# Optimization experiments

Hardware: AMD Instinct MI355X
Metric: run time of the kernel (lower is better)

Reference implementation:

```python
import jax, jax.numpy as jnp
import numpy as np

N_NODES = 50000
N_EDGES = 800000
D_FEAT = 64


def setup_inputs() -> dict:
    key = jax.random.key(0)
    k1, k2, k3 = jax.random.split(key, 3)
    x_sum = jax.random.normal(k1, (N_NODES, D_FEAT), dtype=jnp.float32)
    x_prod = jax.random.uniform(k2, (N_NODES, D_FEAT), dtype=jnp.float32)
    edge_index = jax.random.randint(k3, (2, N_EDGES), 0, N_NODES, dtype=jnp.int64)
    return {"x_sum": x_sum, "x_prod": x_prod, "edge_index": edge_index}


def reference(x_sum, x_prod, edge_index):
    # flow='source_to_target' -> gather from edge_index[0], aggregate at edge_index[1]
    src_idx = edge_index[0]
    dst_idx = edge_index[1]
    n = x_sum.shape[0]

    # __lift__: index_select along node dim (message is identity; edge_attr/norm None)
    m_sum = x_sum[src_idx]    # [E, D]
    m_prod = x_prod[src_idx]  # [E, D]

    # scatter_sum: zeros-init + scatter_add_
    out_sum = jax.ops.segment_sum(m_sum, dst_idx, num_segments=n)

    # scatter_product: ones-init + scatter_(reduce='multiply')
    out_prod = jnp.ones((n, x_prod.shape[1]), dtype=x_prod.dtype).at[dst_idx].multiply(m_prod)

    return out_sum, out_prod
```

## Files before the change

kernel.cpp:

```cpp
#include <hip/hip_runtime.h>
#include <hip/hip_fp16.h>

#define N_NODES 50000
#define N_EDGES 800000
#define D_FEAT  64
#define BSHIFT  6
#define NBKT    782
#define NB      256
#define CHUNK   3125
#define PSHIFT  20
#define SRC_MASK ((1 << PSHIFT) - 1)

#define WS_FLAG    0
#define WS_TOT     64
#define WS_COFF    (WS_TOT + NBKT)
#define WS_BH      (WS_COFF + NBKT + 1)
#define WS_OFFS    (WS_BH + NBKT * NB)
#define WS_PAIR    (WS_OFFS + N_NODES + 1)
#define WS_SSRC    (WS_PAIR + N_EDGES)
#define WS_PACKED  (WS_SSRC + N_EDGES)
#define WS_INTS    (WS_PACKED + N_NODES * D_FEAT)

__device__ inline void detect_idx_layout(const int* idx, int* flag) {
    int allzero = 1;
    #pragma unroll
    for (int i = 1; i < 129; i += 2) {
        if (idx[i] != 0) allzero = 0;
    }
    *flag = allzero;
}

__global__ __launch_bounds__(256) void init_cast(int* __restrict__ W,
                                                 const int* __restrict__ idx,
                                                 const float* __restrict__ xs,
                                                 const float* __restrict__ xp) {
    int tid = blockIdx.x * blockDim.x + threadIdx.x;
    int stride = gridDim.x * blockDim.x;
    __half2* packed = (__half2*)(W + WS_PACKED);
    const int total = N_NODES * D_FEAT;
    for (int i = tid; i < total; i += stride)
        packed[i] = __floats2half2_rn(xs[i], xp[i]);
    if (tid == 0) {
        detect_idx_layout(idx, W + WS_FLAG);
        W[WS_OFFS + N_NODES] = N_EDGES;
    }
}

__global__ __launch_bounds__(256) void block_hist(const int* __restrict__ idx,
                                                  int* __restrict__ W) {
    __shared__ int h[NBKT];
    for (int i = threadIdx.x; i < NBKT; i += 256) h[i] = 0;
    __syncthreads();
    const int flg = W[WS_FLAG];
    const int base = blockIdx.x * CHUNK;
    for (int e = base + threadIdx.x; e < base + CHUNK; e += 256) {
        int dst = flg ? idx[2 * (N_EDGES + e)] : idx[N_EDGES + e];
        atomicAdd(&h[dst >> BSHIFT], 1);
    }
    __syncthreads();
    for (int i = threadIdx.x; i < NBKT; i += 256)
        W[WS_BH + i * NB + blockIdx.x] = h[i];
}

__global__ __launch_bounds__(256) void bucket_scan(int* __restrict__ W) {
    __shared__ int part[NB];
    int j = blockIdx.x;
    int t = threadIdx.x;
    int c = W[WS_BH + j * NB + t];
    part[t] = c;
    __syncthreads();
    for (int off = 1; off < NB; off <<= 1) {
        int u = (t >= off) ? part[t - off] : 0;
        __syncthreads();
        part[t] += u;
        __syncthreads();
    }
    W[WS_BH + j * NB + t] = part[t] - c;
    if (t == NB - 1) W[WS_TOT + j] = part[t];
}

__global__ __launch_bounds__(1024) void base_scan(int* __restrict__ W) {
    __shared__ int part[1024];
    int t = threadIdx.x;
    int v = (t < NBKT) ? W[WS_TOT + t] : 0;
    part[t] = v;
    __syncthreads();
    for (int off = 1; off < 1024; off <<= 1) {
        int u = (t >= off) ? part[t - off] : 0;
        __syncthreads();
        part[t] += u;
        __syncthreads();
    }
    if (t < NBKT) W[WS_COFF + t] = part[t] - v;
    if (t == 0) W[WS_COFF + NBKT] = N_EDGES;
}

__global__ __launch_bounds__(256) void coarse_scatter(const int* __restrict__ idx,
                                                      int* __restrict__ W) {
    __shared__ int cur[NBKT];
    for (int i = threadIdx.x; i < NBKT; i += 256)
        cur[i] = W[WS_COFF + i] + W[WS_BH + i * NB + blockIdx.x];
    __syncthreads();
    const int flg = W[WS_FLAG];
    const int base = blockIdx.x * CHUNK;
    for (int e = base + threadIdx.x; e < base + CHUNK; e += 256) {
        int src, dst;
        if (flg) { src = idx[2 * e]; dst = idx[2 * (N_EDGES + e)]; }
        else     { src = idx[e];     dst = idx[N_EDGES + e]; }
        int pos = atomicAdd(&cur[dst >> BSHIFT], 1);
        W[WS_PAIR + pos] = src | ((dst & 63) << PSHIFT);
    }
}

__global__ __launch_bounds__(256) void fine_sort(int* __restrict__ W) {
    __shared__ int h[64];
    int b = blockIdx.x;
    int t = threadIdx.x;
    int bbase = W[WS_COFF + b];
    int bend  = W[WS_COFF + b + 1];
    if (t < 64) h[t] = 0;
    __syncthreads();
    for (int e = bbase + t; e < bend; e += 256)
        atomicAdd(&h[(unsigned)W[WS_PAIR + e] >> PSHIFT], 1);
    __syncthreads();
    if (t < 64) {
        int c = h[t];
        int incl = c;
        #pragma unroll
        for (int off = 1; off < 64; off <<= 1) {
            int u = __shfl_up(incl, off, 64);
            if (t >= off) incl += u;
        }
        int excl = incl - c;
        int node = (b << BSHIFT) + t;
        if (node < N_NODES) W[WS_OFFS + node] = bbase + excl;
        h[t] = excl;
    }
    __syncthreads();
    for (int e = bbase + t; e < bend; e += 256) {
        int v = W[WS_PAIR + e];
        int p = atomicAdd(&h[(unsigned)v >> PSHIFT], 1);
        W[WS_SSRC + bbase + p] = v & SRC_MASK;
    }
}

__global__ __launch_bounds__(256) void gather_reduce(const int* __restrict__ W,
                                                     float* __restrict__ out) {
    int wave = (int)((blockIdx.x * blockDim.x + threadIdx.x) >> 6);
    int lane = threadIdx.x & 63;
    if (wave >= N_NODES) return;
    int beg = __builtin_amdgcn_readfirstlane(W[WS_OFFS + wave]);
    int end = __builtin_amdgcn_readfirstlane(W[WS_OFFS + wave + 1]);
    const int* ssrc = W + WS_SSRC;
    const __half2* packed = (const __half2*)(W + WS_PACKED);

    float s0 = 0.f, s1 = 0.f, s2 = 0.f, s3 = 0.f;
    float s4 = 0.f, s5 = 0.f, s6 = 0.f, s7 = 0.f;
    float p0 = 1.f, p1 = 1.f, p2 = 1.f, p3 = 1.f;
    float p4 = 1.f, p5 = 1.f, p6 = 1.f, p7 = 1.f;
    int i = beg;
    for (; i + 7 < end; i += 8) {
        int a0 = ssrc[i],     a1 = ssrc[i + 1], a2 = ssrc[i + 2], a3 = ssrc[i + 3];
        int a4 = ssrc[i + 4], a5 = ssrc[i + 5], a6 = ssrc[i + 6], a7 = ssrc[i + 7];
        float2 f0 = __half22float2(packed[a0 * D_FEAT + lane]);
        float2 f1 = __half22float2(packed[a1 * D_FEAT + lane]);
        float2 f2 = __half22float2(packed[a2 * D_FEAT + lane]);
        float2 f3 = __half22float2(packed[a3 * D_FEAT + lane]);
        float2 f4 = __half22float2(packed[a4 * D_FEAT + lane]);
        float2 f5 = __half22float2(packed[a5 * D_FEAT + lane]);
        float2 f6 = __half22float2(packed[a6 * D_FEAT + lane]);
        float2 f7 = __half22float2(packed[a7 * D_FEAT + lane]);
        s0 += f0.x; s1 += f1.x; s2 += f2.x; s3 += f3.x;
        s4 += f4.x; s5 += f5.x; s6 += f6.x; s7 += f7.x;
        p0 *= f0.y; p1 *= f1.y; p2 *= f2.y; p3 *= f3.y;
        p4 *= f4.y; p5 *= f5.y; p6 *= f6.y; p7 *= f7.y;
    }
    for (; i + 1 < end; i += 2) {
        int a0 = ssrc[i], a1 = ssrc[i + 1];
        float2 f0 = __half22float2(packed[a0 * D_FEAT + lane]);
        float2 f1 = __half22float2(packed[a1 * D_FEAT + lane]);
        s0 += f0.x; s1 += f1.x;
        p0 *= f0.y; p1 *= f1.y;
    }
    if (i < end) {
        float2 f = __half22float2(packed[ssrc[i] * D_FEAT + lane]);
        s0 += f.x;
        p0 *= f.y;
    }
    float ssum = ((s0 + s1) + (s2 + s3)) + ((s4 + s5) + (s6 + s7));
    float pprd = ((p0 * p1) * (p2 * p3)) * ((p4 * p5) * (p6 * p7));
    out[(long)wave * D_FEAT + lane] = ssum;
    out[(long)N_NODES * D_FEAT + (long)wave * D_FEAT + lane] = pprd;
}

__device__ inline void atomicMulF32(float* addr, float val) {
    unsigned int* ua = (unsigned int*)addr;
    unsigned int old = __hip_atomic_load(ua, __ATOMIC_RELAXED, __HIP_MEMORY_SCOPE_AGENT);
    while (true) {
        unsigned int assumed = old;
        unsigned int desired = __float_as_uint(__uint_as_float(assumed) * val);
        old = atomicCAS(ua, assumed, desired);
        if (old == assumed) break;
    }
}

__global__ void fb_init(float* __restrict__ out, int* __restrict__ flag,
                        const int* __restrict__ idx) {
    const int n4 = (N_NODES * D_FEAT) / 4;
    int tid = blockIdx.x * blockDim.x + threadIdx.x;
    int stride = gridDim.x * blockDim.x;
    float4* o = (float4*)out;
    const float4 z = make_float4(0.f, 0.f, 0.f, 0.f);
    const float4 one = make_float4(1.f, 1.f, 1.f, 1.f);
    for (int i = tid; i < n4; i += stride) { o[i] = z; o[n4 + i] = one; }
    if (blockIdx.x == 0 && threadIdx.x == 0) detect_idx_layout(idx, flag);
}

__global__ void fb_scatter(const float* __restrict__ xs, const float* __restrict__ xp,
                           const int* __restrict__ idx, float* __restrict__ out,
                           const int* __restrict__ flag) {
    long tid = (long)blockIdx.x * blockDim.x + threadIdx.x;
    const long total = (long)N_EDGES * (D_FEAT / 4);
    if (tid >= total) return;
    int e = (int)(tid >> 4);
    int c = (int)(tid & 15);
    int src, dst;
    if (*flag) { src = idx[2 * e]; dst = idx[2 * (N_EDGES + e)]; }
    else       { src = idx[e];     dst = idx[N_EDGES + e]; }
    const float4 s = ((const float4*)(xs + (long)src * D_FEAT))[c];
    const float4 p = ((const float4*)(xp + (long)src * D_FEAT))[c];
    float* os = out + (long)dst * D_FEAT + c * 4;
    float* op = out + (long)N_NODES * D_FEAT + (long)dst * D_FEAT + c * 4;
    atomicAdd(os + 0, s.x); atomicAdd(os + 1, s.y);
    atomicAdd(os + 2, s.z); atomicAdd(os + 3, s.w);
    atomicMulF32(op + 0, p.x); atomicMulF32(op + 1, p.y);
    atomicMulF32(op + 2, p.z); atomicMulF32(op + 3, p.w);
}

extern "C" void kernel_launch(void* const* d_in, const int* in_sizes, int n_in,
                              void* d_out, int out_size, void* d_ws, size_t ws_size,
                              hipStream_t stream) {
    const float* x_sum  = (const float*)d_in[0];
    const float* x_prod = (const float*)d_in[1];
    const int*   eidx   = (const int*)d_in[2];
    float* out = (float*)d_out;
    int* W = (int*)d_ws;

    if (ws_size < (size_t)WS_INTS * sizeof(int)) {
        fb_init<<<1024, 256, 0, stream>>>(out, W, eidx);
        const long total = (long)N_EDGES * (D_FEAT / 4);
        int grid = (int)((total + 255) / 256);
        fb_scatter<<<grid, 256, 0, stream>>>(x_sum, x_prod, eidx, out, W);
        return;
    }

    init_cast<<<1024, 256, 0, stream>>>(W, eidx, x_sum, x_prod);
    block_hist<<<NB, 256, 0, stream>>>(eidx, W);
    bucket_scan<<<NBKT, 256, 0, stream>>>(W);
    base_scan<<<1, 1024, 0, stream>>>(W);
    coarse_scatter<<<NB, 256, 0, stream>>>(eidx, W);
    fine_sort<<<NBKT, 256, 0, stream>>>(W);
    gather_reduce<<<(N_NODES + 3) / 4, 256, 0, stream>>>(W, out);
}
```

Baseline: 147.4 us.

## Fuse pipeline stages: cast+histogram, inline bucket scan, sort+gather in LDS

Merges the fp16 packing pass with the bucket histogram (now vectorised with float4 loads), drops the separate base_scan kernel by recomputing the bucket prefix inside coarse_scatter and sort_gather, and fuses fine sorting with the gather-reduce so each bucket's sorted source list stays in shared memory. This removes three kernel launches and a global round trip for the sorted indices and node offsets. In exchange, the cast now runs on only 256 blocks, sort_gather redundantly sums bucket totals per block, and buckets larger than CAP fall back to a slower unrolled-free global path.

```diff
diff --git a/kernel.cpp b/kernel.cpp
--- a/kernel.cpp
+++ b/kernel.cpp
@@ -10,16 +10,14 @@
 #define CHUNK   3125
 #define PSHIFT  20
 #define SRC_MASK ((1 << PSHIFT) - 1)
-
-#define WS_FLAG    0
-#define WS_TOT     64
-#define WS_COFF    (WS_TOT + NBKT)
-#define WS_BH      (WS_COFF + NBKT + 1)
-#define WS_OFFS    (WS_BH + NBKT * NB)
-#define WS_PAIR    (WS_OFFS + N_NODES + 1)
-#define WS_SSRC    (WS_PAIR + N_EDGES)
-#define WS_PACKED  (WS_SSRC + N_EDGES)
-#define WS_INTS    (WS_PACKED + N_NODES * D_FEAT)
+#define CAP     6144
+
+#define WS_TOT    0
+#define WS_BH     784
+#define WS_PAIR   (WS_BH + NBKT * NB)
+#define WS_SSRC   (WS_PAIR + N_EDGES)
+#define WS_PACKED (WS_SSRC + N_EDGES)
+#define WS_INTS   (WS_PACKED + N_NODES * D_FEAT)
 
 __device__ inline void detect_idx_layout(const int* idx, int* flag) {
     int allzero = 1;
@@ -30,35 +28,39 @@
     *flag = allzero;
 }
 
-__global__ __launch_bounds__(256) void init_cast(int* __restrict__ W,
+__global__ __launch_bounds__(256) void cast_hist(int* __restrict__ W,
                                                  const int* __restrict__ idx,
                                                  const float* __restrict__ xs,
                                                  const float* __restrict__ xp) {
-    int tid = blockIdx.x * blockDim.x + threadIdx.x;
-    int stride = gridDim.x * blockDim.x;
-    __half2* packed = (__half2*)(W + WS_PACKED);
-    const int total = N_NODES * D_FEAT;
-    for (int i = tid; i < total; i += stride)
-        packed[i] = __floats2half2_rn(xs[i], xp[i]);
-    if (tid == 0) {
-        detect_idx_layout(idx, W + WS_FLAG);
-        W[WS_OFFS + N_NODES] = N_EDGES;
-    }
-}
-
-__global__ __launch_bounds__(256) void block_hist(const int* __restrict__ idx,
-                                                  int* __restrict__ W) {
     __shared__ int h[NBKT];
-    for (int i = threadIdx.x; i < NBKT; i += 256) h[i] = 0;
-    __syncthreads();
-    const int flg = W[WS_FLAG];
+    __shared__ int flg_s;
+    const int t = threadIdx.x;
+    for (int i = t; i < NBKT; i += 256) h[i] = 0;
+    if (t == 0) detect_idx_layout(idx, &flg_s);
+    __syncthreads();
+
+    const float4* xs4 = (const float4*)xs;
+    const float4* xp4 = (const float4*)xp;
+    uint4* pk4 = (uint4*)(W + WS_PACKED);
+    union { __half2 h2; unsigned int u; } c0, c1, c2, c3;
+    const int tid = blockIdx.x * 256 + t;
+    for (int g = tid; g < (N_NODES * D_FEAT) / 4; g += NB * 256) {
+        float4 a = xs4[g], b = xp4[g];
+        c0.h2 = __floats2half2_rn(a.x, b.x);
+        c1.h2 = __floats2half2_rn(a.y, b.y);
+        c2.h2 = __floats2half2_rn(a.z, b.z);
+        c3.h2 = __floats2half2_rn(a.w, b.w);
+        pk4[g] = make_uint4(c0.u, c1.u, c2.u, c3.u);
+    }
+
+    const int flg = flg_s;
     const int base = blockIdx.x * CHUNK;
-    for (int e = base + threadIdx.x; e < base + CHUNK; e += 256) {
+    for (int e = base + t; e < base + CHUNK; e += 256) {
         int dst = flg ? idx[2 * (N_EDGES + e)] : idx[N_EDGES + e];
         atomicAdd(&h[dst >> BSHIFT], 1);
     }
     __syncthreads();
-    for (int i = threadIdx.x; i < NBKT; i += 256)
+    for (int i = t; i < NBKT; i += 256)
         W[WS_BH + i * NB + blockIdx.x] = h[i];
 }
 
@@ -79,31 +81,44 @@
     if (t == NB - 1) W[WS_TOT + j] = part[t];
 }
 
-__global__ __launch_bounds__(1024) void base_scan(int* __restrict__ W) {
-    __shared__ int part[1024];
-    int t = threadIdx.x;
-    int v = (t < NBKT) ? W[WS_TOT + t] : 0;
-    part[t] = v;
-    __syncthreads();
-    for (int off = 1; off < 1024; off <<= 1) {
-        int u = (t >= off) ? part[t - off] : 0;
-        __syncthreads();
-        part[t] += u;
-        __syncthreads();
-    }
-    if (t < NBKT) W[WS_COFF + t] = part[t] - v;
-    if (t == 0) W[WS_COFF + NBKT] = N_EDGES;
-}
-
 __global__ __launch_bounds__(256) void coarse_scatter(const int* __restrict__ idx,
                                                       int* __restrict__ W) {
     __shared__ int cur[NBKT];
-    for (int i = threadIdx.x; i < NBKT; i += 256)
-        cur[i] = W[WS_COFF + i] + W[WS_BH + i * NB + blockIdx.x];
-    __syncthreads();
-    const int flg = W[WS_FLAG];
+    __shared__ int flg_s;
+    const int t = threadIdx.x;
+    for (int i = t; i < NBKT; i += 256) cur[i] = W[WS_TOT + i];
+    if (t == 0) detect_idx_layout(idx, &flg_s);
+    __syncthreads();
+    if (t < 64) {
+        int vals[13];
+        int sum = 0;
+        const int base = t * 13;
+        #pragma unroll
+        for (int j = 0; j < 13; ++j) {
+            int k = base + j;
+            vals[j] = (k < NBKT) ? cur[k] : 0;
+            sum += vals[j];
+        }
+        int incl = sum;
+        #pragma unroll
+        for (int off = 1; off < 64; off <<= 1) {
+            int u = __shfl_up(incl, off, 64);
+            if (t >= off) incl += u;
+        }
+        int run = incl - sum;
+        #pragma unroll
+        for (int j = 0; j < 13; ++j) {
+            int k = base + j;
+            if (k < NBKT) cur[k] = run;
+            run += vals[j];
+        }
+    }
+    __syncthreads();
+    for (int i = t; i < NBKT; i += 256) cur[i] += W[WS_BH + i * NB + blockIdx.x];
+    __syncthreads();
+    const int flg = flg_s;
     const int base = blockIdx.x * CHUNK;
-    for (int e = base + threadIdx.x; e < base + CHUNK; e += 256) {
+    for (int e = base + t; e < base + CHUNK; e += 256) {
         int src, dst;
         if (flg) { src = idx[2 * e]; dst = idx[2 * (N_EDGES + e)]; }
         else     { src = idx[e];     dst = idx[N_EDGES + e]; }
@@ -112,15 +127,30 @@
     }
 }
 
-__global__ __launch_bounds__(256) void fine_sort(int* __restrict__ W) {
+__global__ __launch_bounds__(512) void sort_gather(int* __restrict__ W,
+                                                   float* __restrict__ out) {
+    __shared__ int ssrc_l[CAP];
+    __shared__ int red[512];
     __shared__ int h[64];
-    int b = blockIdx.x;
-    int t = threadIdx.x;
-    int bbase = W[WS_COFF + b];
-    int bend  = W[WS_COFF + b + 1];
+    __shared__ int noff[65];
+    const int b = blockIdx.x;
+    const int t = threadIdx.x;
+
+    int part = 0;
+    for (int k = t; k < b; k += 512) part += W[WS_TOT + k];
+    red[t] = part;
     if (t < 64) h[t] = 0;
     __syncthreads();
-    for (int e = bbase + t; e < bend; e += 256)
+    #pragma unroll
+    for (int off = 256; off > 0; off >>= 1) {
+        if (t < off) red[t] += red[t + off];
+        __syncthreads();
+    }
+    const int bbase = red[0];
+    const int bend  = bbase + W[WS_TOT + b];
+    const int nedge = bend - bbase;
+
+    for (int e = bbase + t; e < bend; e += 512)
         atomicAdd(&h[(unsigned)W[WS_PAIR + e] >> PSHIFT], 1);
     __syncthreads();
     if (t < 64) {
@@ -131,66 +161,86 @@
             int u = __shfl_up(incl, off, 64);
             if (t >= off) incl += u;
         }
-        int excl = incl - c;
-        int node = (b << BSHIFT) + t;
-        if (node < N_NODES) W[WS_OFFS + node] = bbase + excl;
-        h[t] = excl;
-    }
-    __syncthreads();
-    for (int e = bbase + t; e < bend; e += 256) {
-        int v = W[WS_PAIR + e];
-        int p = atomicAdd(&h[(unsigned)v >> PSHIFT], 1);
-        W[WS_SSRC + bbase + p] = v & SRC_MASK;
-    }
-}
-
-__global__ __launch_bounds__(256) void gather_reduce(const int* __restrict__ W,
-                                                     float* __restrict__ out) {
-    int wave = (int)((blockIdx.x * blockDim.x + threadIdx.x) >> 6);
-    int lane = threadIdx.x & 63;
-    if (wave >= N_NODES) return;
-    int beg = __builtin_amdgcn_readfirstlane(W[WS_OFFS + wave]);
-    int end = __builtin_amdgcn_readfirstlane(W[WS_OFFS + wave + 1]);
-    const int* ssrc = W + WS_SSRC;
+        noff[t] = incl - c;
+        if (t == 63) noff[64] = incl;
+        h[t] = incl - c;
+    }
+    __syncthreads();
+
+    const bool fits = (nedge <= CAP);
+    if (fits) {
+        for (int e = bbase + t; e < bend; e += 512) {
+            int v = W[WS_PAIR + e];
+            int p = atomicAdd(&h[(unsigned)v >> PSHIFT], 1);
+            ssrc_l[p] = v & SRC_MASK;
+        }
+    } else {
+        for (int e = bbase + t; e < bend; e += 512) {
+            int v = W[WS_PAIR + e];
+            int p = atomicAdd(&h[(unsigned)v >> PSHIFT], 1);
+            W[WS_SSRC + bbase + p] = v & SRC_MASK;
+        }
+    }
+    __syncthreads();
+
     const __half2* packed = (const __half2*)(W + WS_PACKED);
-
-    float s0 = 0.f, s1 = 0.f, s2 = 0.f, s3 = 0.f;
-    float s4 = 0.f, s5 = 0.f, s6 = 0.f, s7 = 0.f;
-    float p0 = 1.f, p1 = 1.f, p2 = 1.f, p3 = 1.f;
-    float p4 = 1.f, p5 = 1.f, p6 = 1.f, p7 = 1.f;
-    int i = beg;
-    for (; i + 7 < end; i += 8) {
-        int a0 = ssrc[i],     a1 = ssrc[i + 1], a2 = ssrc[i + 2], a3 = ssrc[i + 3];
-        int a4 = ssrc[i + 4], a5 = ssrc[i + 5], a6 = ssrc[i + 6], a7 = ssrc[i + 7];
-        float2 f0 = __half22float2(packed[a0 * D_FEAT + lane]);
-        float2 f1 = __half22float2(packed[a1 * D_FEAT + lane]);
-        float2 f2 = __half22float2(packed[a2 * D_FEAT + lane]);
-        float2 f3 = __half22float2(packed[a3 * D_FEAT + lane]);
-        float2 f4 = __half22float2(packed[a4 * D_FEAT + lane]);
-        float2 f5 = __half22float2(packed[a5 * D_FEAT + lane]);
-        float2 f6 = __half22float2(packed[a6 * D_FEAT + lane]);
-        float2 f7 = __half22float2(packed[a7 * D_FEAT + lane]);
-        s0 += f0.x; s1 += f1.x; s2 += f2.x; s3 += f3.x;
-        s4 += f4.x; s5 += f5.x; s6 += f6.x; s7 += f7.x;
-        p0 *= f0.y; p1 *= f1.y; p2 *= f2.y; p3 *= f3.y;
-        p4 *= f4.y; p5 *= f5.y; p6 *= f6.y; p7 *= f7.y;
-    }
-    for (; i + 1 < end; i += 2) {
-        int a0 = ssrc[i], a1 = ssrc[i + 1];
-        float2 f0 = __half22float2(packed[a0 * D_FEAT + lane]);
-        float2 f1 = __half22float2(packed[a1 * D_FEAT + lane]);
-        s0 += f0.x; s1 += f1.x;
-        p0 *= f0.y; p1 *= f1.y;
-    }
-    if (i < end) {
-        float2 f = __half22float2(packed[ssrc[i] * D_FEAT + lane]);
-        s0 += f.x;
-        p0 *= f.y;
-    }
-    float ssum = ((s0 + s1) + (s2 + s3)) + ((s4 + s5) + (s6 + s7));
-    float pprd = ((p0 * p1) * (p2 * p3)) * ((p4 * p5) * (p6 * p7));
-    out[(long)wave * D_FEAT + lane] = ssum;
-    out[(long)N_NODES * D_FEAT + (long)wave * D_FEAT + lane] = pprd;
+    const int wave = t >> 6;
+    const int lane = t & 63;
+    for (int nn = wave; nn < 64; nn += 8) {
+        const int node = (b << BSHIFT) + nn;
+        if (node >= N_NODES) break;
+        int beg = __builtin_amdgcn_readfirstlane(noff[nn]);
+        int end = __builtin_amdgcn_readfirstlane(noff[nn + 1]);
+
+        float s0 = 0.f, s1 = 0.f, s2 = 0.f, s3 = 0.f;
+        float s4 = 0.f, s5 = 0.f, s6 = 0.f, s7 = 0.f;
+        float p0 = 1.f, p1 = 1.f, p2 = 1.f, p3 = 1.f;
+        float p4 = 1.f, p5 = 1.f, p6 = 1.f, p7 = 1.f;
+        if (fits) {
+            int i = beg;
+            for (; i + 7 < end; i += 8) {
+                int a0 = ssrc_l[i],     a1 = ssrc_l[i + 1];
+                int a2 = ssrc_l[i + 2], a3 = ssrc_l[i + 3];
+                int a4 = ssrc_l[i + 4], a5 = ssrc_l[i + 5];
+                int a6 = ssrc_l[i + 6], a7 = ssrc_l[i + 7];
+                float2 f0 = __half22float2(packed[a0 * D_FEAT + lane]);
+                float2 f1 = __half22float2(packed[a1 * D_FEAT + lane]);
+                float2 f2 = __half22float2(packed[a2 * D_FEAT + lane]);
+                float2 f3 = __half22float2(packed[a3 * D_FEAT + lane]);
+                float2 f4 = __half22float2(packed[a4 * D_FEAT + lane]);
+                float2 f5 = __half22float2(packed[a5 * D_FEAT + lane]);
+                float2 f6 = __half22float2(packed[a6 * D_FEAT + lane]);
+                float2 f7 = __half22float2(packed[a7 * D_FEAT + lane]);
+                s0 += f0.x; s1 += f1.x; s2 += f2.x; s3 += f3.x;
+                s4 += f4.x; s5 += f5.x; s6 += f6.x; s7 += f7.x;
+                p0 *= f0.y; p1 *= f1.y; p2 *= f2.y; p3 *= f3.y;
+                p4 *= f4.y; p5 *= f5.y; p6 *= f6.y; p7 *= f7.y;
+            }
+            for (; i + 1 < end; i += 2) {
+                int a0 = ssrc_l[i], a1 = ssrc_l[i + 1];
+                float2 f0 = __half22float2(packed[a0 * D_FEAT + lane]);
+                float2 f1 = __half22float2(packed[a1 * D_FEAT + lane]);
+                s0 += f0.x; s1 += f1.x;
+                p0 *= f0.y; p1 *= f1.y;
+            }
+            if (i < end) {
+                float2 f = __half22float2(packed[ssrc_l[i] * D_FEAT + lane]);
+                s0 += f.x;
+                p0 *= f.y;
+            }
+        } else {
+            for (int i = beg; i < end; ++i) {
+                int a = W[WS_SSRC + bbase + i];
+                float2 f = __half22float2(packed[a * D_FEAT + lane]);
+                s0 += f.x;
+                p0 *= f.y;
+            }
+        }
+        float ssum = ((s0 + s1) + (s2 + s3)) + ((s4 + s5) + (s6 + s7));
+        float pprd = ((p0 * p1) * (p2 * p3)) * ((p4 * p5) * (p6 * p7));
+        out[(long)node * D_FEAT + lane] = ssum;
+        out[(long)N_NODES * D_FEAT + (long)node * D_FEAT + lane] = pprd;
+    }
 }
 
 __device__ inline void atomicMulF32(float* addr, float val) {
@@ -254,11 +304,8 @@
         return;
     }
 
-    init_cast<<<1024, 256, 0, stream>>>(W, eidx, x_sum, x_prod);
-    block_hist<<<NB, 256, 0, stream>>>(eidx, W);
+    cast_hist<<<NB, 256, 0, stream>>>(W, eidx, x_sum, x_prod);
     bucket_scan<<<NBKT, 256, 0, stream>>>(W);
-    base_scan<<<1, 1024, 0, stream>>>(W);
     coarse_scatter<<<NB, 256, 0, stream>>>(eidx, W);
-    fine_sort<<<NBKT, 256, 0, stream>>>(W);
-    gather_reduce<<<(N_NODES + 3) / 4, 256, 0, stream>>>(W, out);
-}
+    sort_gather<<<NBKT, 512, 0, stream>>>(W, out);
+}
```

Result: faster. 142.3 us (-3.4%).

## Replace multi-pass counting sort with fixed-capacity per-node bucket lists

Applied to the files above, without the earlier changes.

Drops the six-kernel two-level counting sort. The new first kernel appends each edge's source into a fixed 64-slot slot array for its destination node, using global atomics, with an overflow list for nodes past capacity. It also fuses the fp16 packing of both feature tensors into that kernel with vectorized loads. The gather kernel reads each node's source list with one load per lane and broadcasts entries by shuffle, then applies overflow edges with atomics. This cuts launches and passes over the edge list, at the cost of global atomic contention, a larger workspace, nondeterministic edge order, and a slow atomic path if nodes overflow.

```diff
diff --git a/kernel.cpp b/kernel.cpp
--- a/kernel.cpp
+++ b/kernel.cpp
@@ -4,22 +4,20 @@
 #define N_NODES 50000
 #define N_EDGES 800000
 #define D_FEAT  64
-#define BSHIFT  6
-#define NBKT    782
-#define NB      256
-#define CHUNK   3125
-#define PSHIFT  20
-#define SRC_MASK ((1 << PSHIFT) - 1)
-
-#define WS_FLAG    0
-#define WS_TOT     64
-#define WS_COFF    (WS_TOT + NBKT)
-#define WS_BH      (WS_COFF + NBKT + 1)
-#define WS_OFFS    (WS_BH + NBKT * NB)
-#define WS_PAIR    (WS_OFFS + N_NODES + 1)
-#define WS_SSRC    (WS_PAIR + N_EDGES)
-#define WS_PACKED  (WS_SSRC + N_EDGES)
-#define WS_INTS    (WS_PACKED + N_NODES * D_FEAT)
+#define NCAP    64
+
+#define WS_NCNT   0
+#define WS_OVFC   N_NODES
+#define WS_NSRT   (N_NODES + 16)
+#define WS_OVF    (WS_NSRT + N_NODES * NCAP)
+#define WS_PACKED (WS_OVF + 2 * N_EDGES)
+#define WS_INTS   (WS_PACKED + N_NODES * D_FEAT)
+
+#define K1_NB 2048
+#define K1_TH 256
+#define K2_TH 256
+#define NPW   4
+#define K2_NB (N_NODES / ((K2_TH / 64) * NPW))
 
 __device__ inline void detect_idx_layout(const int* idx, int* flag) {
     int allzero = 1;
@@ -30,167 +28,132 @@
     *flag = allzero;
 }
 
-__global__ __launch_bounds__(256) void init_cast(int* __restrict__ W,
-                                                 const int* __restrict__ idx,
-                                                 const float* __restrict__ xs,
-                                                 const float* __restrict__ xp) {
-    int tid = blockIdx.x * blockDim.x + threadIdx.x;
-    int stride = gridDim.x * blockDim.x;
-    __half2* packed = (__half2*)(W + WS_PACKED);
-    const int total = N_NODES * D_FEAT;
-    for (int i = tid; i < total; i += stride)
-        packed[i] = __floats2half2_rn(xs[i], xp[i]);
-    if (tid == 0) {
-        detect_idx_layout(idx, W + WS_FLAG);
-        W[WS_OFFS + N_NODES] = N_EDGES;
-    }
-}
-
-__global__ __launch_bounds__(256) void block_hist(const int* __restrict__ idx,
-                                                  int* __restrict__ W) {
-    __shared__ int h[NBKT];
-    for (int i = threadIdx.x; i < NBKT; i += 256) h[i] = 0;
+__global__ __launch_bounds__(K1_TH) void prep(int* __restrict__ W,
+                                              const int* __restrict__ idx,
+                                              const float* __restrict__ xs,
+                                              const float* __restrict__ xp) {
+    __shared__ int flg_s;
+    if (threadIdx.x == 0) detect_idx_layout(idx, &flg_s);
     __syncthreads();
-    const int flg = W[WS_FLAG];
-    const int base = blockIdx.x * CHUNK;
-    for (int e = base + threadIdx.x; e < base + CHUNK; e += 256) {
-        int dst = flg ? idx[2 * (N_EDGES + e)] : idx[N_EDGES + e];
-        atomicAdd(&h[dst >> BSHIFT], 1);
-    }
-    __syncthreads();
-    for (int i = threadIdx.x; i < NBKT; i += 256)
-        W[WS_BH + i * NB + blockIdx.x] = h[i];
-}
-
-__global__ __launch_bounds__(256) void bucket_scan(int* __restrict__ W) {
-    __shared__ int part[NB];
-    int j = blockIdx.x;
-    int t = threadIdx.x;
-    int c = W[WS_BH + j * NB + t];
-    part[t] = c;
-    __syncthreads();
-    for (int off = 1; off < NB; off <<= 1) {
-        int u = (t >= off) ? part[t - off] : 0;
+    const int flg = flg_s;
+    const int tid = blockIdx.x * K1_TH + threadIdx.x;
+    const int nthr = K1_NB * K1_TH;
+
+    const float4* xs4 = (const float4*)xs;
+    const float4* xp4 = (const float4*)xp;
+    uint4* pk4 = (uint4*)(W + WS_PACKED);
+    for (int g = tid; g < (N_NODES * D_FEAT) / 4; g += nthr) {
+        float4 a = xs4[g], p = xp4[g];
+        union { __half2 h2; unsigned int u; } c0, c1, c2, c3;
+        c0.h2 = __floats2half2_rn(a.x, p.x);
+        c1.h2 = __floats2half2_rn(a.y, p.y);
+        c2.h2 = __floats2half2_rn(a.z, p.z);
+        c3.h2 = __floats2half2_rn(a.w, p.w);
+        pk4[g] = make_uint4(c0.u, c1.u, c2.u, c3.u);
+    }
+
+    for (int e = tid; e < N_EDGES; e += nthr) {
+        int s, d;
+        if (flg) {
+            s = ((const int2*)idx)[e].x;
+            d = ((const int2*)idx)[N_EDGES + e].x;
+        } else {
+            s = idx[e];
+            d = idx[N_EDGES + e];
+        }
+        int pos = atomicAdd(&W[WS_NCNT + d], 1);
+        if (pos < NCAP) {
+            W[WS_NSRT + d * NCAP + pos] = s;
+        } else {
+            int op = atomicAdd(&W[WS_OVFC], 1);
+            W[WS_OVF + 2 * op]     = d;
+            W[WS_OVF + 2 * op + 1] = s;
+        }
+    }
+}
+
+__global__ __launch_bounds__(K2_TH) void gather(const int* __restrict__ W,
+                                                float* __restrict__ out) {
+    const int wave = threadIdx.x >> 6;
+    const int lane = threadIdx.x & 63;
+    const __half2* packed = (const __half2*)(W + WS_PACKED);
+    const int* nsrt = W + WS_NSRT;
+    const int nbase = blockIdx.x * ((K2_TH / 64) * NPW) + wave * NPW;
+
+    #pragma unroll
+    for (int i = 0; i < NPW; ++i) {
+        const int node = nbase + i;
+        int cnt = __builtin_amdgcn_readfirstlane(W[WS_NCNT + node]);
+        if (cnt > NCAP) cnt = NCAP;
+        const int* sp = nsrt + node * NCAP;
+        int mysrc = (lane < cnt) ? sp[lane] : 0;
+
+        float s0 = 0.f, s1 = 0.f, s2 = 0.f, s3 = 0.f;
+        float s4 = 0.f, s5 = 0.f, s6 = 0.f, s7 = 0.f;
+        float p0 = 1.f, p1 = 1.f, p2 = 1.f, p3 = 1.f;
+        float p4 = 1.f, p5 = 1.f, p6 = 1.f, p7 = 1.f;
+        int j = 0;
+        for (; j + 7 < cnt; j += 8) {
+            int a0 = __shfl(mysrc, j + 0), a1 = __shfl(mysrc, j + 1);
+            int a2 = __shfl(mysrc, j + 2), a3 = __shfl(mysrc, j + 3);
+            int a4 = __shfl(mysrc, j + 4), a5 = __shfl(mysrc, j + 5);
+            int a6 = __shfl(mysrc, j + 6), a7 = __shfl(mysrc, j + 7);
+            float2 f0 = __half22float2(packed[a0 * D_FEAT + lane]);
+            float2 f1 = __half22float2(packed[a1 * D_FEAT + lane]);
+            float2 f2 = __half22float2(packed[a2 * D_FEAT + lane]);
+            float2 f3 = __half22float2(packed[a3 * D_FEAT + lane]);
+            float2 f4 = __half22float2(packed[a4 * D_FEAT + lane]);
+            float2 f5 = __half22float2(packed[a5 * D_FEAT + lane]);
+            float2 f6 = __half22float2(packed[a6 * D_FEAT + lane]);
+            float2 f7 = __half22float2(packed[a7 * D_FEAT + lane]);
+            s0 += f0.x; s1 += f1.x; s2 += f2.x; s3 += f3.x;
+            s4 += f4.x; s5 += f5.x; s6 += f6.x; s7 += f7.x;
+            p0 *= f0.y; p1 *= f1.y; p2 *= f2.y; p3 *= f3.y;
+            p4 *= f4.y; p5 *= f5.y; p6 *= f6.y; p7 *= f7.y;
+        }
+        for (; j + 1 < cnt; j += 2) {
+            int a0 = __shfl(mysrc, j), a1 = __shfl(mysrc, j + 1);
+            float2 f0 = __half22float2(packed[a0 * D_FEAT + lane]);
+            float2 f1 = __half22float2(packed[a1 * D_FEAT + lane]);
+            s0 += f0.x; s1 += f1.x;
+            p0 *= f0.y; p1 *= f1.y;
+        }
+        if (j < cnt) {
+            float2 f = __half22float2(packed[__shfl(mysrc, j) * D_FEAT + lane]);
+            s0 += f.x;
+            p0 *= f.y;
+        }
+        float ssum = ((s0 + s1) + (s2 + s3)) + ((s4 + s5) + (s6 + s7));
+        float pprd = ((p0 * p1) * (p2 * p3)) * ((p4 * p5) * (p6 * p7));
+        out[(long)node * D_FEAT + lane] = ssum;
+        out[(long)N_NODES * D_FEAT + (long)node * D_FEAT + lane] = pprd;
+    }
+
+    int novf = __builtin_amdgcn_readfirstlane(W[WS_OVFC]);
+    if (novf > 0) {
         __syncthreads();
-        part[t] += u;
-        __syncthreads();
-    }
-    W[WS_BH + j * NB + t] = part[t] - c;
-    if (t == NB - 1) W[WS_TOT + j] = part[t];
-}
-
-__global__ __launch_bounds__(1024) void base_scan(int* __restrict__ W) {
-    __shared__ int part[1024];
-    int t = threadIdx.x;
-    int v = (t < NBKT) ? W[WS_TOT + t] : 0;
-    part[t] = v;
-    __syncthreads();
-    for (int off = 1; off < 1024; off <<= 1) {
-        int u = (t >= off) ? part[t - off] : 0;
-        __syncthreads();
-        part[t] += u;
-        __syncthreads();
-    }
-    if (t < NBKT) W[WS_COFF + t] = part[t] - v;
-    if (t == 0) W[WS_COFF + NBKT] = N_EDGES;
-}
-
-__global__ __launch_bounds__(256) void coarse_scatter(const int* __restrict__ idx,
-                                                      int* __restrict__ W) {
-    __shared__ int cur[NBKT];
-    for (int i = threadIdx.x; i < NBKT; i += 256)
-        cur[i] = W[WS_COFF + i] + W[WS_BH + i * NB + blockIdx.x];
-    __syncthreads();
-    const int flg = W[WS_FLAG];
-    const int base = blockIdx.x * CHUNK;
-    for (int e = base + threadIdx.x; e < base + CHUNK; e += 256) {
-        int src, dst;
-        if (flg) { src = idx[2 * e]; dst = idx[2 * (N_EDGES + e)]; }
-        else     { src = idx[e];     dst = idx[N_EDGES + e]; }
-        int pos = atomicAdd(&cur[dst >> BSHIFT], 1);
-        W[WS_PAIR + pos] = src | ((dst & 63) << PSHIFT);
-    }
-}
-
-__global__ __launch_bounds__(256) void fine_sort(int* __restrict__ W) {
-    __shared__ int h[64];
-    int b = blockIdx.x;
-    int t = threadIdx.x;
-    int bbase = W[WS_COFF + b];
-    int bend  = W[WS_COFF + b + 1];
-    if (t < 64) h[t] = 0;
-    __syncthreads();
-    for (int e = bbase + t; e < bend; e += 256)
-        atomicAdd(&h[(unsigned)W[WS_PAIR + e] >> PSHIFT], 1);
-    __syncthreads();
-    if (t < 64) {
-        int c = h[t];
-        int incl = c;
-        #pragma unroll
-        for (int off = 1; off < 64; off <<= 1) {
-            int u = __shfl_up(incl, off, 64);
-            if (t >= off) incl += u;
-        }
-        int excl = incl - c;
-        int node = (b << BSHIFT) + t;
-        if (node < N_NODES) W[WS_OFFS + node] = bbase + excl;
-        h[t] = excl;
-    }
-    __syncthreads();
-    for (int e = bbase + t; e < bend; e += 256) {
-        int v = W[WS_PAIR + e];
-        int p = atomicAdd(&h[(unsigned)v >> PSHIFT], 1);
-        W[WS_SSRC + bbase + p] = v & SRC_MASK;
-    }
-}
-
-__global__ __launch_bounds__(256) void gather_reduce(const int* __restrict__ W,
-                                                     float* __restrict__ out) {
-    int wave = (int)((blockIdx.x * blockDim.x + threadIdx.x) >> 6);
-    int lane = threadIdx.x & 63;
-    if (wave >= N_NODES) return;
-    int beg = __builtin_amdgcn_readfirstlane(W[WS_OFFS + wave]);
-    int end = __builtin_amdgcn_readfirstlane(W[WS_OFFS + wave + 1]);
-    const int* ssrc = W + WS_SSRC;
-    const __half2* packed = (const __half2*)(W + WS_PACKED);
-
-    float s0 = 0.f, s1 = 0.f, s2 = 0.f, s3 = 0.f;
-    float s4 = 0.f, s5 = 0.f, s6 = 0.f, s7 = 0.f;
-    float p0 = 1.f, p1 = 1.f, p2 = 1.f, p3 = 1.f;
-    float p4 = 1.f, p5 = 1.f, p6 = 1.f, p7 = 1.f;
-    int i = beg;
-    for (; i + 7 < end; i += 8) {
-        int a0 = ssrc[i],     a1 = ssrc[i + 1], a2 = ssrc[i + 2], a3 = ssrc[i + 3];
-        int a4 = ssrc[i + 4], a5 = ssrc[i + 5], a6 = ssrc[i + 6], a7 = ssrc[i + 7];
-        float2 f0 = __half22float2(packed[a0 * D_FEAT + lane]);
-        float2 f1 = __half22float2(packed[a1 * D_FEAT + lane]);
-        float2 f2 = __half22float2(packed[a2 * D_FEAT + lane]);
-        float2 f3 = __half22float2(packed[a3 * D_FEAT + lane]);
-        float2 f4 = __half22float2(packed[a4 * D_FEAT + lane]);
-        float2 f5 = __half22float2(packed[a5 * D_FEAT + lane]);
-        float2 f6 = __half22float2(packed[a6 * D_FEAT + lane]);
-        float2 f7 = __half22float2(packed[a7 * D_FEAT + lane]);
-        s0 += f0.x; s1 += f1.x; s2 += f2.x; s3 += f3.x;
-        s4 += f4.x; s5 += f5.x; s6 += f6.x; s7 += f7.x;
-        p0 *= f0.y; p1 *= f1.y; p2 *= f2.y; p3 *= f3.y;
-        p4 *= f4.y; p5 *= f5.y; p6 *= f6.y; p7 *= f7.y;
-    }
-    for (; i + 1 < end; i += 2) {
-        int a0 = ssrc[i], a1 = ssrc[i + 1];
-        float2 f0 = __half22float2(packed[a0 * D_FEAT + lane]);
-        float2 f1 = __half22float2(packed[a1 * D_FEAT + lane]);
-        s0 += f0.x; s1 += f1.x;
-        p0 *= f0.y; p1 *= f1.y;
-    }
-    if (i < end) {
-        float2 f = __half22float2(packed[ssrc[i] * D_FEAT + lane]);
-        s0 += f.x;
-        p0 *= f.y;
-    }
-    float ssum = ((s0 + s1) + (s2 + s3)) + ((s4 + s5) + (s6 + s7));
-    float pprd = ((p0 * p1) * (p2 * p3)) * ((p4 * p5) * (p6 * p7));
-    out[(long)wave * D_FEAT + lane] = ssum;
-    out[(long)N_NODES * D_FEAT + (long)wave * D_FEAT + lane] = pprd;
+        for (int k = wave; k < novf; k += (K2_TH / 64)) {
+            int d = W[WS_OVF + 2 * k];
+            if (d >= nbase - wave * NPW &&
+                d < nbase - wave * NPW + (K2_TH / 64) * NPW) {
+                int s = W[WS_OVF + 2 * k + 1];
+                float2 f = __half22float2(packed[s * D_FEAT + lane]);
+                float* os = out + (long)d * D_FEAT + lane;
+                float* op = out + (long)N_NODES * D_FEAT + (long)d * D_FEAT + lane;
+                atomicAdd(os, f.x);
+                unsigned int* ua = (unsigned int*)op;
+                unsigned int old = __hip_atomic_load(ua, __ATOMIC_RELAXED,
+                                                     __HIP_MEMORY_SCOPE_AGENT);
+                while (true) {
+                    unsigned int assumed = old;
+                    unsigned int desired =
+                        __float_as_uint(__uint_as_float(assumed) * f.y);
+                    old = atomicCAS(ua, assumed, desired);
+                    if (old == assumed) break;
+                }
+            }
+        }
+    }
 }
 
 __device__ inline void atomicMulF32(float* addr, float val) {
@@ -254,11 +217,7 @@
         return;
     }
 
-    init_cast<<<1024, 256, 0, stream>>>(W, eidx, x_sum, x_prod);
-    block_hist<<<NB, 256, 0, stream>>>(eidx, W);
-    bucket_scan<<<NBKT, 256, 0, stream>>>(W);
-    base_scan<<<1, 1024, 0, stream>>>(W);
-    coarse_scatter<<<NB, 256, 0, stream>>>(eidx, W);
-    fine_sort<<<NBKT, 256, 0, stream>>>(W);
-    gather_reduce<<<(N_NODES + 3) / 4, 256, 0, stream>>>(W, out);
-}
+    hipMemsetAsync(W, 0, (size_t)(N_NODES + 1) * sizeof(int), stream);
+    prep<<<K1_NB, K1_TH, 0, stream>>>(W, eidx, x_sum, x_prod);
+    gather<<<K2_NB, K2_TH, 0, stream>>>(W, out);
+}
```

New measurement: 180.1 us. +22.2%, slower.
